# Kernel optimization log

Measured on AMD Instinct MI355X. Metric: run time of the kernel, lower is better.

## Reference

```python
import jax, jax.numpy as jnp
import numpy as np

EPS = 1e-5

def mesh_conv(x, gemm, W, b):
    # x: [B,C,E], gemm: [B,E,5] int32 (col 0 = self, cols 1..4 = neighbors)
    f = jax.vmap(lambda xb, gb: xb[:, gb])(x, gemm)  # [B,C,E,5] gather
    g = jnp.stack([
        f[..., 0],
        f[..., 1] + f[..., 3],
        f[..., 2] + f[..., 4],
        jnp.abs(f[..., 1] - f[..., 3]),
        jnp.abs(f[..., 2] - f[..., 4]),
    ], axis=-1)                                      # symmetric GeMM features
    # Conv2d kernel (1,5) == contraction over (C, 5)
    return jnp.einsum('bcek,ock->boe', g, W) + b[None, :, None]

def instance_norm(x):
    # InstanceNorm2d(affine=False): per-(b,c) biased normalization over edges
    mu = jnp.mean(x, axis=2, keepdims=True)
    var = jnp.mean((x - mu) ** 2, axis=2, keepdims=True)
    return (x - mu) * jax.lax.rsqrt(var + EPS)

def setup_inputs():
    key = jax.random.key(0)
    ks = jax.random.split(key, 8)
    B, Cin, Cout, Ein, Eout = 2, 256, 128, 4500, 9000
    from_up = jax.random.normal(ks[0], (B, Cin, Ein), jnp.float32)
    from_down = jax.random.normal(ks[1], (B, Cout, Eout), jnp.float32)
    gemm_up = jax.random.randint(ks[2], (B, Ein, 5), 0, Ein, jnp.int32)
    gemm_post = jax.random.randint(ks[3], (B, Eout, 5), 0, Eout, jnp.int32)
    # MeshUnpool matrix: each input edge splits into 2 output edges, occ=1
    parent = np.arange(Eout) // 2
    mat = np.zeros((Ein, Eout), np.float32)
    mat[parent, np.arange(Eout)] = 1.0
    unroll_mat = jnp.broadcast_to(jnp.asarray(mat), (B, Ein, Eout))
    W_up = jax.random.normal(ks[4], (Cout, Cin, 5), jnp.float32) * 0.02
    b_up = jnp.zeros((Cout,), jnp.float32)
    W1 = jax.random.normal(ks[5], (Cout, 2 * Cout, 5), jnp.float32) * 0.02
    b1 = jnp.zeros((Cout,), jnp.float32)
    W2 = jax.random.normal(ks[6], (Cout, Cout, 5), jnp.float32) * 0.02
    b2 = jnp.zeros((Cout,), jnp.float32)
    return dict(from_up=from_up, from_down=from_down, unroll_mat=unroll_mat,
                W_up=W_up, b_up=b_up, W1=W1, b1=b1, W2=W2, b2=b2,
                gemm_up=gemm_up, gemm_post=gemm_post)

def reference(from_up, from_down, unroll_mat, W_up, b_up, W1, b1, W2, b2,
              gemm_up, gemm_post):
    x1 = mesh_conv(from_up, gemm_up, W_up, b_up)       # up_conv -> [B,Cout,Ein]
    x1 = jnp.einsum('bce,beo->bco', x1, unroll_mat)    # MeshUnpool -> [B,Cout,Eout]
    x1 = jnp.concatenate([x1, from_down], axis=1)      # transfer_data skip cat
    x1 = mesh_conv(x1, gemm_post, W1, b1)              # conv1
    x1 = jax.nn.relu(instance_norm(x1))
    x2 = mesh_conv(x1, gemm_post, W2, b2)              # conv2[0]
    x2 = jax.nn.relu(instance_norm(x2) + x1)           # residual + relu
    return x2
```

## Files before the change

### kernel.cpp

```cpp
#include <hip/hip_runtime.h>
#include <hip/hip_bf16.h>
#include <math.h>

#define NB 2
#define EIN 4500
#define EOUT 9000
#define EPS 1e-5f

typedef __attribute__((ext_vector_type(8))) short bf16x8;
typedef __attribute__((ext_vector_type(4))) float f32x4;

__device__ inline uint32_t bfr(float x) {
    uint32_t u = __float_as_uint(x);
    return (u + 0x7fffu + ((u >> 16) & 1u)) >> 16;
}
__device__ inline uint32_t pk2(float a, float b) {
    __hip_bfloat162 h = __float22bfloat162_rn(make_float2(a, b));
    uint32_t u;
    __builtin_memcpy(&u, &h, 4);
    return u;
}
__device__ inline float bf2f(ushort u) { return __uint_as_float((uint32_t)u << 16); }

__device__ inline void wpack_frag(const float* __restrict__ W, ushort* __restrict__ Wq,
                                  int i, int CIN) {
    int lane = i & 63; int t = i >> 6;
    int ot = t & 1; t >>= 1;
    int ks = t & 3; t >>= 2;
    int NCH = CIN / 16;
    int ch = t % NCH, w = t / NCH;
    int o = w * 32 + ot * 16 + (lane & 15);
    int c = ch * 16 + ks * 4 + (lane >> 4);
    const float* src = W + ((size_t)o * CIN + c) * 5;
    uint4 v;
    v.x = pk2(src[0], src[1]);
    v.y = pk2(src[2], src[3]);
    v.z = pk2(src[4], 0.f);
    v.w = 0u;
    *reinterpret_cast<uint4*>(Wq + (size_t)i * 8) = v;
}

__device__ inline void transpose_bf_body(float (*tile)[33], const float* __restrict__ in,
                                         ushort* __restrict__ out, int R, int C,
                                         int id, int nbx, int nby, int tid) {
    int bxt = id % nbx; int rest = id / nbx;
    int by = rest % nby; int b = rest / nby;
    int c0 = bxt * 32, r0 = by * 32;
    const float* inb = in + (size_t)b * R * C;
    ushort* outb = out + (size_t)b * C * R;
    int tx = tid & 31, ty = tid >> 5;
#pragma unroll
    for (int i = 0; i < 4; ++i) {
        int r = r0 + ty + i * 8, c = c0 + tx;
        if (r < R && c < C) tile[ty + i * 8][tx] = inb[(size_t)r * C + c];
    }
    __syncthreads();
#pragma unroll
    for (int i = 0; i < 4; ++i) {
        int c = c0 + ty + i * 8, r = r0 + tx;
        if (r < R && c < C) outb[(size_t)c * R + r] = (ushort)bfr(tile[tx][ty + i * 8]);
    }
}

#define GUESS_B 71
#define FU_B 2256
#define FD_B 2256
#define WP_B 320
#define INIT_B 1
__global__ __launch_bounds__(256) void phase0_kernel(
    const float* __restrict__ unroll, int* __restrict__ parent, float* __restrict__ pval,
    const float* __restrict__ from_up, ushort* __restrict__ FU,
    const float* __restrict__ from_down, ushort* __restrict__ FD,
    const float* __restrict__ W_up, ushort* __restrict__ Wq_up,
    const float* __restrict__ W1, ushort* __restrict__ Wq_1,
    const float* __restrict__ W2, ushort* __restrict__ Wq_2,
    float* __restrict__ stats) {
    __shared__ float tile[32][33];
    int bx = blockIdx.x, tid = threadIdx.x;
    if (bx < GUESS_B) {
        int i = bx * 256 + tid;
        if (i < NB * EOUT) {
            int eo = i % EOUT;
            const float* mb = unroll + (size_t)(i / EOUT) * EIN * EOUT;
            int p = eo >> 1;
            float v = mb[(size_t)p * EOUT + eo];
            if (v == 0.f) {
                p = 0; v = 0.f;
                for (int ei = 0; ei < EIN; ++ei) {
                    float x = mb[(size_t)ei * EOUT + eo];
                    if (x != 0.f) { p = ei; v = x; break; }
                }
            }
            parent[i] = p;
            pval[i] = v;
        }
    } else if (bx < GUESS_B + FU_B) {
        transpose_bf_body(tile, from_up, FU, 256, EIN, bx - GUESS_B, 141, 8, tid);
    } else if (bx < GUESS_B + FU_B + FD_B) {
        transpose_bf_body(tile, from_down, FD, 128, EOUT, bx - (GUESS_B + FU_B), 282, 4, tid);
    } else if (bx < GUESS_B + FU_B + FD_B + WP_B) {
        int i = (bx - (GUESS_B + FU_B + FD_B)) * 256 + tid;
        if (i < 32768) wpack_frag(W_up, Wq_up, i, 256);
        else if (i < 65536) wpack_frag(W1, Wq_1, i - 32768, 256);
        else wpack_frag(W2, Wq_2, i - 65536, 128);
    } else {
#pragma unroll
        for (int j = 0; j < 4; ++j) stats[j * 256 + tid] = 0.f;
    }
}

template <int CIN, int MODE, bool STATS>
__global__ __launch_bounds__(512, 4) void conv_mfma(
    const ushort* __restrict__ Xs, const ushort* __restrict__ Aux,
    const int* __restrict__ gm, const int* __restrict__ parent,
    const float* __restrict__ pval, const float* __restrict__ stats_in,
    const ushort* __restrict__ Wq, const float* __restrict__ bias,
    ushort* __restrict__ Out, float* __restrict__ stats_out, int E) {
    constexpr int NCH16 = CIN / 16;
    constexpr int NCH = CIN / 32;
    constexpr int LDW = 264;
    constexpr int GSZ = 64 * LDW;
    __shared__ __align__(16) ushort Gs[2 * GSZ];
    __shared__ int idx[320];
    __shared__ int par[MODE == 1 ? 320 : 1];
    __shared__ float pv[MODE == 1 ? 320 : 1];
    __shared__ float muS[MODE == 2 ? 128 : 1];
    __shared__ float rinvS[MODE == 2 ? 128 : 1];

    int tid = threadIdx.x;
    int b = blockIdx.y, e0 = blockIdx.x * 64;

    if (tid < 320) {
        int e = tid / 5, k = tid % 5;
        int eg = e0 + e;
        int id = (eg < E) ? gm[((size_t)b * E + eg) * 5 + k] : 0;
        idx[tid] = id;
        if (MODE == 1) {
            par[tid] = parent[b * EOUT + id];
            pv[tid] = pval[b * EOUT + id];
        }
    }
    if (MODE == 2 && tid < 128) {
        float s = stats_in[(b * 128 + tid) * 2 + 0];
        float q = stats_in[(b * 128 + tid) * 2 + 1];
        float invE = 1.0f / (float)EOUT;
        float mu = s * invE;
        muS[tid] = mu;
        rinvS[tid] = rsqrtf(q * invE - mu * mu + EPS);
    }
    __syncthreads();

    int l = tid & 63, w = tid >> 6;
    int lr = l & 15, lg = l >> 4;
    int cg = tid & 7, eb = tid >> 3;
    bool evalid = (e0 + eb) < E;
    constexpr int XROW = (MODE == 0) ? CIN : 128;

    f32x4 acc[4];
#pragma unroll
    for (int et = 0; et < 4; ++et) acc[et] = (f32x4)0.f;

    uint2 g[5];
    auto loadG = [&](int chu) {
        int c0 = chu * 32 + cg * 4;
#pragma unroll
        for (int k = 0; k < 5; ++k) {
            g[k] = make_uint2(0u, 0u);
            if (evalid) {
                int s5 = eb * 5 + k;
                const ushort* src;
                if (MODE == 1) {
                    if (chu < NCH / 2) src = Xs + ((size_t)b * EIN + par[s5]) * 128 + c0;
                    else src = Aux + ((size_t)b * EOUT + idx[s5]) * 128 + (c0 - 128);
                } else {
                    src = Xs + ((size_t)b * E + idx[s5]) * XROW + c0;
                }
                g[k] = *reinterpret_cast<const uint2*>(src);
            }
        }
    };

    auto stageG = [&](int chu, ushort* gbuf) {
        float pvr[5];
        if (MODE == 1 && chu < NCH / 2) {
#pragma unroll
            for (int k = 0; k < 5; ++k) pvr[k] = pv[eb * 5 + k];
        }
#pragma unroll
        for (int j = 0; j < 4; ++j) {
            float f[5];
#pragma unroll
            for (int k = 0; k < 5; ++k) {
                uint32_t word = (j < 2) ? g[k].x : g[k].y;
                ushort h = (j & 1) ? (ushort)(word >> 16) : (ushort)(word & 0xffff);
                f[k] = bf2f(h);
            }
            if (MODE == 1 && chu < NCH / 2) {
#pragma unroll
                for (int k = 0; k < 5; ++k) f[k] *= pvr[k];
            } else if (MODE == 2) {
                int c = chu * 32 + cg * 4 + j;
                float mu = muS[c], rinv = rinvS[c];
#pragma unroll
                for (int k = 0; k < 5; ++k) {
                    float z = (f[k] - mu) * rinv;
                    f[k] = z > 0.f ? z : 0.f;
                }
            }
            uint4 v;
            v.x = pk2(f[0], f[1] + f[3]);
            v.y = pk2(f[2] + f[4], fabsf(f[1] - f[3]));
            v.z = pk2(fabsf(f[2] - f[4]), 0.f);
            v.w = 0u;
            *reinterpret_cast<uint4*>(gbuf + eb * LDW + (cg * 4 + j) * 8) = v;
        }
    };

    loadG(0);
    for (int chu = 0; chu < NCH; ++chu) {
        ushort* gbuf = Gs + (chu & 1) * GSZ;
        stageG(chu, gbuf);
        __syncthreads();
        if (chu + 1 < NCH) loadG(chu + 1);
#pragma unroll
        for (int ks = 0; ks < 8; ++ks) {
            int ch16 = chu * 2 + (ks >> 2), ksl = ks & 3;
            const ushort* wbase =
                Wq + ((size_t)(((((w >> 1) * NCH16 + ch16) * 4 + ksl) * 2 + (w & 1)) * 64 + l)) * 8;
            bf16x8 bb = *reinterpret_cast<const bf16x8*>(wbase);
#pragma unroll
            for (int et = 0; et < 4; ++et) {
                bf16x8 a = *reinterpret_cast<const bf16x8*>(
                    gbuf + (et * 16 + lr) * LDW + ks * 32 + lg * 8);
                acc[et] = __builtin_amdgcn_mfma_f32_16x16x32_bf16(a, bb, acc[et], 0, 0, 0);
            }
        }
    }

    {
        int o = w * 16 + lr;
        float bv = bias[o];
        float s = 0.f, q = 0.f;
#pragma unroll
        for (int et = 0; et < 4; ++et) {
#pragma unroll
            for (int r = 0; r < 4; ++r) {
                int e = e0 + et * 16 + lg * 4 + r;
                if (e < E) {
                    float y = acc[et][r] + bv;
                    Out[((size_t)b * E + e) * 128 + o] = (ushort)bfr(y);
                    if (STATS) { s += y; q += y * y; }
                }
            }
        }
        if (STATS) {
            s += __shfl_xor(s, 16, 64); s += __shfl_xor(s, 32, 64);
            q += __shfl_xor(q, 16, 64); q += __shfl_xor(q, 32, 64);
            if (lg == 0) {
                atomicAdd(&stats_out[(b * 128 + o) * 2 + 0], s);
                atomicAdd(&stats_out[(b * 128 + o) * 2 + 1], q);
            }
        }
    }
}

__global__ void final_kernel(const ushort* __restrict__ Y3, const ushort* __restrict__ Y2,
                             const float* __restrict__ stats1, const float* __restrict__ stats2,
                             float* __restrict__ out, int E) {
    __shared__ float tile[32 * 129];
    int b = blockIdx.y;
    int e0 = blockIdx.x * 32;
    int tid = threadIdx.x;
    float invE = 1.0f / (float)E;
#pragma unroll
    for (int i = 0; i < 16; ++i) {
        int idx = i * 256 + tid;
        int c = idx & 127, el = idx >> 7;
        int e = e0 + el;
        float v = 0.f;
        if (e < E) {
            float s1 = stats1[(b * 128 + c) * 2 + 0], q1 = stats1[(b * 128 + c) * 2 + 1];
            float mu1 = s1 * invE, var1 = q1 * invE - mu1 * mu1;
            float s2 = stats2[(b * 128 + c) * 2 + 0], q2 = stats2[(b * 128 + c) * 2 + 1];
            float mu2 = s2 * invE, var2 = q2 * invE - mu2 * mu2;
            float x1 = (bf2f(Y2[((size_t)b * E + e) * 128 + c]) - mu1) * rsqrtf(var1 + EPS);
            x1 = x1 > 0.f ? x1 : 0.f;
            float z = (bf2f(Y3[((size_t)b * E + e) * 128 + c]) - mu2) * rsqrtf(var2 + EPS);
            v = z + x1;
            v = v > 0.f ? v : 0.f;
        }
        tile[el * 129 + c] = v;
    }
    __syncthreads();
#pragma unroll
    for (int i = 0; i < 16; ++i) {
        int idx = i * 256 + tid;
        int el = idx & 31, c = idx >> 5;
        int e = e0 + el;
        if (e < E) out[((size_t)b * 128 + c) * E + e] = tile[el * 129 + c];
    }
}

extern "C" void kernel_launch(void* const* d_in, const int* in_sizes, int n_in,
                              void* d_out, int out_size, void* d_ws, size_t ws_size,
                              hipStream_t stream) {
    const float* from_up   = (const float*)d_in[0];
    const float* from_down = (const float*)d_in[1];
    const float* unroll    = (const float*)d_in[2];
    const float* W_up      = (const float*)d_in[3];
    const float* b_up      = (const float*)d_in[4];
    const float* W1        = (const float*)d_in[5];
    const float* b1        = (const float*)d_in[6];
    const float* W2        = (const float*)d_in[7];
    const float* b2        = (const float*)d_in[8];
    const int* gemm_up     = (const int*)d_in[9];
    const int* gemm_post   = (const int*)d_in[10];
    float* out = (float*)d_out;

    float* ws = (float*)d_ws;
    size_t off = 0;
    auto alloc = [&](size_t n) { float* p = ws + off; off += n; return p; };
    ushort* FU_bf = (ushort*)alloc((size_t)NB * EIN * 256 / 2);
    ushort* FD_bf = (ushort*)alloc((size_t)NB * EOUT * 128 / 2);
    ushort* Wq_up = (ushort*)alloc(131072);
    ushort* Wq_1  = (ushort*)alloc(131072);
    ushort* Wq_2  = (ushort*)alloc(65536);
    ushort* Y1_bf = (ushort*)alloc((size_t)NB * EIN * 128 / 2);
    ushort* Y2_bf = (ushort*)alloc((size_t)NB * EOUT * 128 / 2);
    ushort* Y3_bf = (ushort*)alloc((size_t)NB * EOUT * 128 / 2);
    float* stats  = alloc(1024);
    int*   parent = (int*)alloc(NB * EOUT);
    float* pval   = alloc(NB * EOUT);
    float* stats1 = stats, *stats2 = stats + 512;

    phase0_kernel<<<GUESS_B + FU_B + FD_B + WP_B + INIT_B, 256, 0, stream>>>(
        unroll, parent, pval, from_up, FU_bf, from_down, FD_bf,
        W_up, Wq_up, W1, Wq_1, W2, Wq_2, stats);

    conv_mfma<256, 0, false><<<dim3(71, NB), 512, 0, stream>>>(
        FU_bf, nullptr, gemm_up, nullptr, nullptr, nullptr, Wq_up, b_up, Y1_bf, nullptr, EIN);
    conv_mfma<256, 1, true><<<dim3(141, NB), 512, 0, stream>>>(
        Y1_bf, FD_bf, gemm_post, parent, pval, nullptr, Wq_1, b1, Y2_bf, stats1, EOUT);
    conv_mfma<128, 2, true><<<dim3(141, NB), 512, 0, stream>>>(
        Y2_bf, nullptr, gemm_post, nullptr, nullptr, stats1, Wq_2, b2, Y3_bf, stats2, EOUT);
    final_kernel<<<dim3(282, NB), 256, 0, stream>>>(Y3_bf, Y2_bf, stats1, stats2, out, EOUT);
}
```

Baseline: 110.3 us.

## Pack GeMM features densely along K to drop zero-padded MFMA steps

```diff
diff --git a/kernel.cpp b/kernel.cpp
--- a/kernel.cpp
+++ b/kernel.cpp
@@ -25,19 +25,19 @@
 __device__ inline void wpack_frag(const float* __restrict__ W, ushort* __restrict__ Wq,
                                   int i, int CIN) {
     int lane = i & 63; int t = i >> 6;
-    int ot = t & 1; t >>= 1;
-    int ks = t & 3; t >>= 2;
-    int NCH = CIN / 16;
-    int ch = t % NCH, w = t / NCH;
-    int o = w * 32 + ot * 16 + (lane & 15);
-    int c = ch * 16 + ks * 4 + (lane >> 4);
-    const float* src = W + ((size_t)o * CIN + c) * 5;
-    uint4 v;
-    v.x = pk2(src[0], src[1]);
-    v.y = pk2(src[2], src[3]);
-    v.z = pk2(src[4], 0.f);
-    v.w = 0u;
-    *reinterpret_cast<uint4*>(Wq + (size_t)i * 8) = v;
+    int NSTEP = CIN * 5 / 32;
+    int st = t % NSTEP, og = t / NSTEP;
+    int o = og * 16 + (lane & 15);
+    int k0 = st * 32 + (lane >> 4) * 8;
+    uint32_t u[4];
+#pragma unroll
+    for (int q = 0; q < 4; ++q) {
+        int ka = k0 + 2 * q, kb = ka + 1;
+        float va = W[((size_t)o * CIN + ka / 5) * 5 + ka % 5];
+        float vb = W[((size_t)o * CIN + kb / 5) * 5 + kb % 5];
+        u[q] = pk2(va, vb);
+    }
+    *reinterpret_cast<uint4*>(Wq + (size_t)i * 8) = make_uint4(u[0], u[1], u[2], u[3]);
 }
 
 __device__ inline void transpose_bf_body(float (*tile)[33], const float* __restrict__ in,
@@ -65,7 +65,7 @@
 #define GUESS_B 71
 #define FU_B 2256
 #define FD_B 2256
-#define WP_B 320
+#define WP_B 200
 #define INIT_B 1
 __global__ __launch_bounds__(256) void phase0_kernel(
     const float* __restrict__ unroll, int* __restrict__ parent, float* __restrict__ pval,
@@ -100,9 +100,9 @@
         transpose_bf_body(tile, from_down, FD, 128, EOUT, bx - (GUESS_B + FU_B), 282, 4, tid);
     } else if (bx < GUESS_B + FU_B + FD_B + WP_B) {
         int i = (bx - (GUESS_B + FU_B + FD_B)) * 256 + tid;
-        if (i < 32768) wpack_frag(W_up, Wq_up, i, 256);
-        else if (i < 65536) wpack_frag(W1, Wq_1, i - 32768, 256);
-        else wpack_frag(W2, Wq_2, i - 65536, 128);
+        if (i < 20480) wpack_frag(W_up, Wq_up, i, 256);
+        else if (i < 40960) wpack_frag(W1, Wq_1, i - 20480, 256);
+        else wpack_frag(W2, Wq_2, i - 40960, 128);
     } else {
 #pragma unroll
         for (int j = 0; j < 4; ++j) stats[j * 256 + tid] = 0.f;
@@ -116,9 +116,9 @@
     const float* __restrict__ pval, const float* __restrict__ stats_in,
     const ushort* __restrict__ Wq, const float* __restrict__ bias,
     ushort* __restrict__ Out, float* __restrict__ stats_out, int E) {
-    constexpr int NCH16 = CIN / 16;
     constexpr int NCH = CIN / 32;
-    constexpr int LDW = 264;
+    constexpr int NSTEP = CIN * 5 / 32;
+    constexpr int LDW = 168;
     constexpr int GSZ = 64 * LDW;
     __shared__ __align__(16) ushort Gs[2 * GSZ];
     __shared__ int idx[320];
@@ -186,6 +186,7 @@
 #pragma unroll
             for (int k = 0; k < 5; ++k) pvr[k] = pv[eb * 5 + k];
         }
+        float fa[20];
 #pragma unroll
         for (int j = 0; j < 4; ++j) {
             float f[5];
@@ -207,13 +208,19 @@
                     f[k] = z > 0.f ? z : 0.f;
                 }
             }
-            uint4 v;
-            v.x = pk2(f[0], f[1] + f[3]);
-            v.y = pk2(f[2] + f[4], fabsf(f[1] - f[3]));
-            v.z = pk2(fabsf(f[2] - f[4]), 0.f);
-            v.w = 0u;
-            *reinterpret_cast<uint4*>(gbuf + eb * LDW + (cg * 4 + j) * 8) = v;
-        }
+            fa[j * 5 + 0] = f[0];
+            fa[j * 5 + 1] = f[1] + f[3];
+            fa[j * 5 + 2] = f[2] + f[4];
+            fa[j * 5 + 3] = fabsf(f[1] - f[3]);
+            fa[j * 5 + 4] = fabsf(f[2] - f[4]);
+        }
+        uint32_t u[10];
+#pragma unroll
+        for (int q = 0; q < 10; ++q) u[q] = pk2(fa[2 * q], fa[2 * q + 1]);
+        ushort* dst = gbuf + eb * LDW + cg * 20;
+#pragma unroll
+        for (int q = 0; q < 5; ++q)
+            *reinterpret_cast<uint2*>(dst + q * 4) = make_uint2(u[2 * q], u[2 * q + 1]);
     };
 
     loadG(0);
@@ -223,10 +230,9 @@
         __syncthreads();
         if (chu + 1 < NCH) loadG(chu + 1);
 #pragma unroll
-        for (int ks = 0; ks < 8; ++ks) {
-            int ch16 = chu * 2 + (ks >> 2), ksl = ks & 3;
+        for (int ks = 0; ks < 5; ++ks) {
             const ushort* wbase =
-                Wq + ((size_t)(((((w >> 1) * NCH16 + ch16) * 4 + ksl) * 2 + (w & 1)) * 64 + l)) * 8;
+                Wq + ((size_t)(w * NSTEP + chu * 5 + ks) * 64 + l) * 8;
             bf16x8 bb = *reinterpret_cast<const bf16x8*>(wbase);
 #pragma unroll
             for (int et = 0; et < 4; ++et) {
@@ -322,9 +328,9 @@
     auto alloc = [&](size_t n) { float* p = ws + off; off += n; return p; };
     ushort* FU_bf = (ushort*)alloc((size_t)NB * EIN * 256 / 2);
     ushort* FD_bf = (ushort*)alloc((size_t)NB * EOUT * 128 / 2);
-    ushort* Wq_up = (ushort*)alloc(131072);
-    ushort* Wq_1  = (ushort*)alloc(131072);
-    ushort* Wq_2  = (ushort*)alloc(65536);
+    ushort* Wq_up = (ushort*)alloc(81920);
+    ushort* Wq_1  = (ushort*)alloc(81920);
+    ushort* Wq_2  = (ushort*)alloc(40960);
     ushort* Y1_bf = (ushort*)alloc((size_t)NB * EIN * 128 / 2);
     ushort* Y2_bf = (ushort*)alloc((size_t)NB * EOUT * 128 / 2);
     ushort* Y3_bf = (ushort*)alloc((size_t)NB * EOUT * 128 / 2);
```

Result: faster. 98.81 us (-10.4%).
